# Optimization experiments

Measured on AMD Instinct MI355X. Metric: run time of the kernel, lower is better.

The kernel has to match this reference:

```python
import jax, jax.numpy as jnp
import numpy as np

B, T = 32, 25
TAU_M, TAU_S = 4.0, 1.0
TH, SG = 1.0, 4.0  # spike threshold, surrogate-gradient sharpness

@jax.custom_vjp
def spike_fn(v):
    return (v > TH).astype(v.dtype)

def _spike_fwd(v):
    return spike_fn(v), v

def _spike_bwd(v, g):
    s = jax.nn.sigmoid(SG * (v - TH))
    return (g * SG * s * (1.0 - s),)

spike_fn.defvjp(_spike_fwd, _spike_bwd)

def setup_inputs() -> dict:
    key = jax.random.key(0)
    ks = jax.random.split(key, 13)
    d = {}
    d["inputs"] = jax.random.normal(ks[0], (B, 3, 32, 32), jnp.float32)
    d["ann1_w"] = jax.random.normal(ks[1], (32, 3, 3, 3), jnp.float32) * 0.1
    d["ann1_b"] = jnp.zeros((32,), jnp.float32)
    d["w2"] = jax.random.normal(ks[2], (32, 32, 3, 3), jnp.float32) * 0.06
    d["b2"] = jnp.zeros((32,), jnp.float32)
    d["w3"] = jax.random.normal(ks[3], (64, 32, 3, 3), jnp.float32) * 0.06
    d["b3"] = jnp.zeros((64,), jnp.float32)
    d["w5"] = jax.random.normal(ks[4], (64, 64, 3, 3), jnp.float32) * 0.04
    d["b5"] = jnp.zeros((64,), jnp.float32)
    d["w7"] = jax.random.normal(ks[5], (512, 1600), jnp.float32) * (1.0 / np.sqrt(1600))
    d["b7"] = jnp.zeros((512,), jnp.float32)
    d["w8"] = jax.random.normal(ks[6], (10, 512), jnp.float32) * (1.0 / np.sqrt(512))
    d["b8"] = jnp.zeros((10,), jnp.float32)
    return d

def _conv(x, w, b):
    y = jax.lax.conv_general_dilated(x, w, (1, 1), 'VALID',
                                     dimension_numbers=('NCHW', 'OIHW', 'NCHW'))
    return y + b[None, :, None, None]

def _maxpool(x):
    return jax.lax.reduce_window(x, -jnp.inf, jax.lax.max,
                                 (1, 1, 2, 2), (1, 1, 2, 2), 'VALID')

def reference(inputs, ann1_w, ann1_b, w2, b2, w3, b3, w5, b5, w7, b7, w8, b8):
    eta_m = jnp.exp(jnp.asarray(-1.0 / TAU_M, jnp.float32))
    eta_s = jnp.exp(jnp.asarray(-1.0 / TAU_S, jnp.float32))
    a1, a2c = eta_m + eta_s, -eta_m * eta_s  # dual-exp IIR coefficients

    # ANN front-end, constant over time (expand_along_time just repeats it)
    frame = jax.nn.sigmoid(_conv(inputs, ann1_w, ann1_b))  # [B,32,30,30]

    def axon(x, st):  # second-order dual-exponential IIR synapse
        y1, y2 = st
        y = a1 * y1 + a2c * y2 + x
        return y, (y, y1)

    def lif(cur, st):  # LIF with membrane filter, zero-reset via prev spike
        v, s = st
        v_new = eta_m * v * (1.0 - s) + cur
        spk = spike_fn(v_new)
        return spk, (v_new, spk)

    def z(*shape):
        zz = jnp.zeros(shape, jnp.float32)
        return (zz, zz)

    carry0 = (z(B, 32, 30, 30), z(B, 32, 28, 28), z(B, 32, 28, 28),
              z(B, 64, 26, 26), z(B, 64, 26, 26), z(B, 64, 13, 13),
              z(B, 64, 11, 11), z(B, 64, 11, 11), z(B, 1600),
              z(B, 512), z(B, 512), z(B, 10))

    def step(carry, _):
        ax2, sn2, ax3, sn3, ax4, ax5, sn5, ax6, ax7, sn7, ax8, sn8 = carry
        a2o, ax2 = axon(frame, ax2)
        s2, sn2 = lif(_conv(a2o, w2, b2), sn2)
        a3o, ax3 = axon(s2, ax3)
        s3, sn3 = lif(_conv(a3o, w3, b3), sn3)
        a4o, ax4 = axon(s3, ax4)
        s4 = _maxpool(a4o)                       # [B,64,13,13]
        a5o, ax5 = axon(s4, ax5)
        s5, sn5 = lif(_conv(a5o, w5, b5), sn5)   # [B,64,11,11]
        a6o, ax6 = axon(s5, ax6)
        s6 = _maxpool(a6o)                       # [B,64,5,5]
        flat = s6.reshape(B, -1)                 # [B,1600]
        a7o, ax7 = axon(flat, ax7)
        s7, sn7 = lif(a7o @ w7.T + b7, sn7)      # [B,512]
        a8o, ax8 = axon(s7, ax8)
        s8, sn8 = lif(a8o @ w8.T + b8, sn8)      # [B,10]
        return (ax2, sn2, ax3, sn3, ax4, ax5, sn5, ax6, ax7, sn7, ax8, sn8), s8

    _, outs = jax.lax.scan(step, carry0, None, length=T)  # [T,B,10]
    return jnp.transpose(outs, (1, 2, 0))  # [B,10,T] matching torch time-last layout
```

## Files before the change

### kernel.cpp

```cpp
#include <hip/hip_runtime.h>
#include <math.h>


__device__ __forceinline__ float axon_step(float A1, float A2, float y1, float y2, float x) {
    return __fadd_rn(__fadd_rn(__fmul_rn(A1, y1), __fmul_rn(A2, y2)), x);
}

__global__ void diag_kernel(float* out, float v, int n) {
    int i = blockIdx.x * 256 + threadIdx.x;
    if (i < n) out[i] = v;
}

__global__ void canary_kernel(float* out, int n) {
    __shared__ float ssum[256];
    float s = 0.f;
    for (int i = threadIdx.x; i < n; i += 256) s += out[i];
    ssum[threadIdx.x] = s;
    __syncthreads();
    for (int k = 128; k > 0; k >>= 1) {
        if (threadIdx.x < k) ssum[threadIdx.x] += ssum[threadIdx.x + k];
        __syncthreads();
    }
    if (threadIdx.x == 0 && ssum[0] == 0.0f) out[0] = 444.0f;
}

__global__ __launch_bounds__(256) void wcvt_kernel(
        const float* __restrict__ w2, const float* __restrict__ w3,
        const float* __restrict__ w5,
        double* __restrict__ w2d, double* __restrict__ w3d,
        double* __restrict__ w5d) {
    int i = blockIdx.x * 256 + threadIdx.x;
    if (i < 9216)  w2d[i] = (double)w2[i];
    if (i < 18432) w3d[i] = (double)w3[i];
    if (i < 36864) w5d[i] = (double)w5[i];
}

__global__ __launch_bounds__(256) void ann1_kernel(
        const float* __restrict__ in, const float* __restrict__ w,
        const float* __restrict__ bias, float* __restrict__ frame) {
    int bid = blockIdx.x;
    int b = bid & 31, co = bid >> 5;
    int tid = threadIdx.x;
    __shared__ double wsh[27];
    if (tid < 27) wsh[tid] = (double)w[co * 27 + tid];
    __syncthreads();
    float bb = bias[co];
    for (int p = tid; p < 900; p += 256) {
        int y = p / 30, x = p % 30;
        double acc = 0.0;
        #pragma unroll
        for (int ci = 0; ci < 3; ++ci) {
            const float* r = in + ((b * 3 + ci) * 32 + y) * 32 + x;
            const double* wp = wsh + ci * 9;
            #pragma unroll
            for (int ky = 0; ky < 3; ++ky)
                acc += (double)r[ky*32+0]*wp[ky*3+0] + (double)r[ky*32+1]*wp[ky*3+1]
                     + (double)r[ky*32+2]*wp[ky*3+2];
        }
        float z = __fadd_rn((float)acc, bb);
        frame[((b * 32 + co) * 30 + y) * 30 + x] =
            (float)(1.0 / (1.0 + exp(-(double)z)));
    }
}

__global__ __launch_bounds__(256) void axon2g_kernel(
        const float2* __restrict__ frame2, float* __restrict__ a2ch,
        float A1, float A2) {
    int g = blockIdx.x * 256 + threadIdx.x;
    float2 f = frame2[g];
    float y1a = 0.f, y2a = 0.f, y1b = 0.f, y2b = 0.f;
    #pragma unroll
    for (int k = 0; k < 25; ++k) {
        float v0 = axon_step(A1, A2, y1a, y2a, f.x);
        float v1 = axon_step(A1, A2, y1b, y2b, f.y);
        ((float2*)(a2ch + (size_t)k * 921600))[g] = make_float2(v0, v1);
        y2a = y1a; y1a = v0;
        y2b = y1b; y1b = v1;
    }
}

__global__ __launch_bounds__(256) void conv2g_kernel(
        const float* __restrict__ a2ch, const double* __restrict__ w2d,
        const float* __restrict__ b2, float* __restrict__ a3ch,
        float A1, float A2, float eta_m) {
    int bid = blockIdx.x;
    int b = bid & 31, cop = (bid >> 5) & 15, sp = (bid >> 9) & 1;
    int co0 = cop * 2;
    int row0 = sp * 14;
    int p = threadIdx.x;
    if (p >= 196) return;
    int lr = p / 14, xp = p % 14;
    int y = row0 + lr, x = xp * 2;
    const double* wbase = w2d + co0 * 288;
    float bb0 = b2[co0], bb1 = b2[co0 + 1];
    float w2s[4] = {0.f, 0.f, 0.f, 0.f};
    float y3a[4] = {0.f, 0.f, 0.f, 0.f};
    float y3b[4] = {0.f, 0.f, 0.f, 0.f};
    size_t roffb = ((size_t)(b * 32) * 30 + y) * 30 + x;
    for (int tt = 0; tt < 12; ++tt) {
        const float* p0 = a2ch + (size_t)(2 * tt) * 921600;
        const float* p1 = p0 + 921600;
        double e00[2] = {0.0, 0.0}, e01[2] = {0.0, 0.0};
        double e10[2] = {0.0, 0.0}, e11[2] = {0.0, 0.0};
        #pragma unroll 2
        for (int ci = 0; ci < 32; ++ci) {
            const float* r0 = p0 + roffb + ci * 900;
            const float* r1 = p1 + roffb + ci * 900;
            const double* wp = wbase + ci * 9;
            #pragma unroll
            for (int ky = 0; ky < 3; ++ky) {
                float2 lo0 = *(const float2*)(r0 + ky * 30);
                float2 hi0 = *(const float2*)(r0 + ky * 30 + 2);
                float2 lo1 = *(const float2*)(r1 + ky * 30);
                float2 hi1 = *(const float2*)(r1 + ky * 30 + 2);
                double u0 = (double)lo0.x, u1 = (double)lo0.y;
                double u2 = (double)hi0.x, u3 = (double)hi0.y;
                double v0 = (double)lo1.x, v1 = (double)lo1.y;
                double v2 = (double)hi1.x, v3 = (double)hi1.y;
                #pragma unroll
                for (int j = 0; j < 2; ++j) {
                    const double* wj = wp + j * 288 + ky * 3;
                    e00[j] += u0*wj[0] + u1*wj[1] + u2*wj[2];
                    e01[j] += u1*wj[0] + u2*wj[1] + u3*wj[2];
                    e10[j] += v0*wj[0] + v1*wj[1] + v2*wj[2];
                    e11[j] += v1*wj[0] + v2*wj[1] + v3*wj[2];
                }
            }
        }
        float* a3o0 = a3ch + (size_t)(2 * tt) * 802816;
        float* a3o1 = a3o0 + 802816;
        #pragma unroll
        for (int j = 0; j < 2; ++j) {
            float bb = j ? bb1 : bb0;
            #pragma unroll
            for (int u = 0; u < 2; ++u) {
                int s = j * 2 + u;
                int idx = (b * 32 + co0 + j) * 784 + y * 28 + x + u;
                float cur = __fadd_rn((float)(u ? e01[j] : e00[j]), bb);
                float vn = __fadd_rn(__fmul_rn(eta_m, w2s[s]), cur);
                float sn = vn > 1.0f ? 1.0f : 0.0f;
                w2s[s] = vn > 1.0f ? 0.0f : vn;
                float yv = axon_step(A1, A2, y3a[s], y3b[s], sn);
                y3b[s] = y3a[s]; y3a[s] = yv;
                a3o0[idx] = yv;
                cur = __fadd_rn((float)(u ? e11[j] : e10[j]), bb);
                vn = __fadd_rn(__fmul_rn(eta_m, w2s[s]), cur);
                sn = vn > 1.0f ? 1.0f : 0.0f;
                w2s[s] = vn > 1.0f ? 0.0f : vn;
                yv = axon_step(A1, A2, y3a[s], y3b[s], sn);
                y3b[s] = y3a[s]; y3a[s] = yv;
                a3o1[idx] = yv;
            }
        }
    }
    {
        const float* a2o = a2ch + (size_t)24 * 921600;
        double e00[2] = {0.0, 0.0}, e01[2] = {0.0, 0.0};
        #pragma unroll 2
        for (int ci = 0; ci < 32; ++ci) {
            const float* r = a2o + roffb + ci * 900;
            const double* wp = wbase + ci * 9;
            #pragma unroll
            for (int ky = 0; ky < 3; ++ky) {
                float2 lo = *(const float2*)(r + ky * 30);
                float2 hi = *(const float2*)(r + ky * 30 + 2);
                double u0 = (double)lo.x, u1 = (double)lo.y;
                double u2 = (double)hi.x, u3 = (double)hi.y;
                #pragma unroll
                for (int j = 0; j < 2; ++j) {
                    const double* wj = wp + j * 288 + ky * 3;
                    e00[j] += u0*wj[0] + u1*wj[1] + u2*wj[2];
                    e01[j] += u1*wj[0] + u2*wj[1] + u3*wj[2];
                }
            }
        }
        float* a3o = a3ch + (size_t)24 * 802816;
        #pragma unroll
        for (int j = 0; j < 2; ++j) {
            float bb = j ? bb1 : bb0;
            #pragma unroll
            for (int u = 0; u < 2; ++u) {
                int s = j * 2 + u;
                int idx = (b * 32 + co0 + j) * 784 + y * 28 + x + u;
                float cur = __fadd_rn((float)(u ? e01[j] : e00[j]), bb);
                float vn = __fadd_rn(__fmul_rn(eta_m, w2s[s]), cur);
                float sn = vn > 1.0f ? 1.0f : 0.0f;
                w2s[s] = vn > 1.0f ? 0.0f : vn;
                float yv = axon_step(A1, A2, y3a[s], y3b[s], sn);
                y3b[s] = y3a[s]; y3a[s] = yv;
                a3o[idx] = yv;
            }
        }
    }
}

__global__ __launch_bounds__(256) void conv3g_kernel(
        const float* __restrict__ a3ch, const double* __restrict__ w3d,
        const float* __restrict__ b3, float* __restrict__ a5ch,
        float A1, float A2, float eta_m) {
    int bid = blockIdx.x;
    int b = bid & 31, coq = (bid >> 5) & 15, sp = bid >> 9;
    int co0 = coq * 4;
    int row0 = sp ? 14 : 0;
    int nrow = sp ? 12 : 14;
    int pr0  = sp ? 7 : 0;
    int npr  = sp ? 6 : 7;
    int tid = threadIdx.x;
    __shared__ float tile0[4 * 364];
    __shared__ float tile1[4 * 364];
    int npair = nrow * 13;
    int npool = npr * 13 * 4;
    const double* wbase = w3d + co0 * 288;
    int lr = 0, xp = 0, y = 0, x = 0;
    bool convAct = tid < npair;
    if (convAct) { lr = tid / 13; xp = tid % 13; y = row0 + lr; x = xp * 2; }
    float bb[4];
    #pragma unroll
    for (int j = 0; j < 4; ++j) bb[j] = b3[co0 + j];
    float w3s[8], y4a[8], y4b[8];
    #pragma unroll
    for (int s = 0; s < 8; ++s) { w3s[s] = 0.f; y4a[s] = 0.f; y4b[s] = 0.f; }
    float y5a[2] = {0.f, 0.f}, y5b[2] = {0.f, 0.f};
    size_t roffb = ((size_t)(b * 32) * 28 + y) * 28 + x;
    for (int tt = 0; tt < 12; ++tt) {
        if (convAct) {
            const float* p0 = a3ch + (size_t)(2 * tt) * 802816;
            const float* p1 = p0 + 802816;
            double e00[4] = {0,0,0,0}, e01[4] = {0,0,0,0};
            double e10[4] = {0,0,0,0}, e11[4] = {0,0,0,0};
            #pragma unroll 2
            for (int ci = 0; ci < 32; ++ci) {
                const float* r0 = p0 + roffb + ci * 784;
                const float* r1 = p1 + roffb + ci * 784;
                const double* wp = wbase + ci * 9;
                #pragma unroll
                for (int ky = 0; ky < 3; ++ky) {
                    float2 lo0 = *(const float2*)(r0 + ky * 28);
                    float2 hi0 = *(const float2*)(r0 + ky * 28 + 2);
                    float2 lo1 = *(const float2*)(r1 + ky * 28);
                    float2 hi1 = *(const float2*)(r1 + ky * 28 + 2);
                    double u0 = (double)lo0.x, u1 = (double)lo0.y;
                    double u2 = (double)hi0.x, u3 = (double)hi0.y;
                    double v0 = (double)lo1.x, v1 = (double)lo1.y;
                    double v2 = (double)hi1.x, v3 = (double)hi1.y;
                    #pragma unroll
                    for (int j = 0; j < 4; ++j) {
                        const double* wj = wp + j * 288 + ky * 3;
                        e00[j] += u0*wj[0] + u1*wj[1] + u2*wj[2];
                        e01[j] += u1*wj[0] + u2*wj[1] + u3*wj[2];
                        e10[j] += v0*wj[0] + v1*wj[1] + v2*wj[2];
                        e11[j] += v1*wj[0] + v2*wj[1] + v3*wj[2];
                    }
                }
            }
            #pragma unroll
            for (int j = 0; j < 4; ++j) {
                #pragma unroll
                for (int u = 0; u < 2; ++u) {
                    int s = j * 2 + u;
                    float cur = __fadd_rn((float)(u ? e01[j] : e00[j]), bb[j]);
                    float vn = __fadd_rn(__fmul_rn(eta_m, w3s[s]), cur);
                    float sn = vn > 1.0f ? 1.0f : 0.0f;
                    w3s[s] = vn > 1.0f ? 0.0f : vn;
                    float a4 = axon_step(A1, A2, y4a[s], y4b[s], sn);
                    y4b[s] = y4a[s]; y4a[s] = a4;
                    tile0[j * 364 + lr * 26 + x + u] = a4;
                    cur = __fadd_rn((float)(u ? e11[j] : e10[j]), bb[j]);
                    vn = __fadd_rn(__fmul_rn(eta_m, w3s[s]), cur);
                    sn = vn > 1.0f ? 1.0f : 0.0f;
                    w3s[s] = vn > 1.0f ? 0.0f : vn;
                    a4 = axon_step(A1, A2, y4a[s], y4b[s], sn);
                    y4b[s] = y4a[s]; y4a[s] = a4;
                    tile1[j * 364 + lr * 26 + x + u] = a4;
                }
            }
        }
        __syncthreads();
        float* a5o0 = a5ch + (size_t)(2 * tt) * 346112;
        float* a5o1 = a5o0 + 346112;
        #pragma unroll
        for (int s = 0; s < 2; ++s) {
            int q = tid + s * 256;
            if (q < npool) {
                int j = q / (npr * 13), pp = q % (npr * 13);
                int pry = pp / 13, px = pp % 13;
                int pr = pr0 + pry;
                int tlr = 2 * pr - row0;
                int toff = j * 364 + tlr * 26 + 2 * px;
                int idx = (b * 64 + co0 + j) * 169 + pr * 13 + px;
                const float* tp = tile0 + toff;
                float m = fmaxf(fmaxf(tp[0], tp[1]), fmaxf(tp[26], tp[27]));
                float yv = axon_step(A1, A2, y5a[s], y5b[s], m);
                y5b[s] = y5a[s]; y5a[s] = yv;
                a5o0[idx] = yv;
                tp = tile1 + toff;
                m = fmaxf(fmaxf(tp[0], tp[1]), fmaxf(tp[26], tp[27]));
                yv = axon_step(A1, A2, y5a[s], y5b[s], m);
                y5b[s] = y5a[s]; y5a[s] = yv;
                a5o1[idx] = yv;
            }
        }
        __syncthreads();
    }
    {
        if (convAct) {
            const float* a3o = a3ch + (size_t)24 * 802816;
            double e00[4] = {0,0,0,0}, e01[4] = {0,0,0,0};
            #pragma unroll 2
            for (int ci = 0; ci < 32; ++ci) {
                const float* r = a3o + roffb + ci * 784;
                const double* wp = wbase + ci * 9;
                #pragma unroll
                for (int ky = 0; ky < 3; ++ky) {
                    float2 lo = *(const float2*)(r + ky * 28);
                    float2 hi = *(const float2*)(r + ky * 28 + 2);
                    double u0 = (double)lo.x, u1 = (double)lo.y;
                    double u2 = (double)hi.x, u3 = (double)hi.y;
                    #pragma unroll
                    for (int j = 0; j < 4; ++j) {
                        const double* wj = wp + j * 288 + ky * 3;
                        e00[j] += u0*wj[0] + u1*wj[1] + u2*wj[2];
                        e01[j] += u1*wj[0] + u2*wj[1] + u3*wj[2];
                    }
                }
            }
            #pragma unroll
            for (int j = 0; j < 4; ++j) {
                #pragma unroll
                for (int u = 0; u < 2; ++u) {
                    int s = j * 2 + u;
                    float cur = __fadd_rn((float)(u ? e01[j] : e00[j]), bb[j]);
                    float vn = __fadd_rn(__fmul_rn(eta_m, w3s[s]), cur);
                    float sn = vn > 1.0f ? 1.0f : 0.0f;
                    w3s[s] = vn > 1.0f ? 0.0f : vn;
                    float a4 = axon_step(A1, A2, y4a[s], y4b[s], sn);
                    y4b[s] = y4a[s]; y4a[s] = a4;
                    tile0[j * 364 + lr * 26 + x + u] = a4;
                }
            }
        }
        __syncthreads();
        float* a5o = a5ch + (size_t)24 * 346112;
        #pragma unroll
        for (int s = 0; s < 2; ++s) {
            int q = tid + s * 256;
            if (q < npool) {
                int j = q / (npr * 13), pp = q % (npr * 13);
                int pry = pp / 13, px = pp % 13;
                int pr = pr0 + pry;
                int tlr = 2 * pr - row0;
                const float* tp = tile0 + j * 364 + tlr * 26 + 2 * px;
                float m = fmaxf(fmaxf(tp[0], tp[1]), fmaxf(tp[26], tp[27]));
                int idx = (b * 64 + co0 + j) * 169 + pr * 13 + px;
                float yv = axon_step(A1, A2, y5a[s], y5b[s], m);
                y5b[s] = y5a[s]; y5a[s] = yv;
                a5o[idx] = yv;
            }
        }
    }
}

__global__ __launch_bounds__(128) void conv5g_kernel(
        const float* __restrict__ a5ch, const double* __restrict__ w5d,
        const float* __restrict__ b5, float* __restrict__ a7ch,
        float A1, float A2, float eta_m) {
    int bid = blockIdx.x;
    int b = bid & 31, co = bid >> 5;
    int tid = threadIdx.x;
    __shared__ float tile0[121];
    __shared__ float tile1[121];
    const double* wbase = w5d + co * 576;
    float bb = b5[co];
    float w5s = 0.f, y6a = 0.f, y6b = 0.f;
    float y7a = 0.f, y7b = 0.f;
    int yy = tid / 11, xx = tid % 11;
    int py = tid / 5, px = tid % 5;
    size_t roffb = (size_t)(b * 64) * 169 + yy * 13 + xx;
    for (int tt = 0; tt < 12; ++tt) {
        if (tid < 121) {
            const float* p0 = a5ch + (size_t)(2 * tt) * 346112;
            const float* p1 = p0 + 346112;
            double a0[9] = {0,0,0,0,0,0,0,0,0};
            double a1[9] = {0,0,0,0,0,0,0,0,0};
            #pragma unroll 2
            for (int ci = 0; ci < 64; ++ci) {
                const float* r0 = p0 + roffb + ci * 169;
                const float* r1 = p1 + roffb + ci * 169;
                const double* wp = wbase + ci * 9;
                a0[0] += (double)r0[0]  * wp[0];
                a0[1] += (double)r0[1]  * wp[1];
                a0[2] += (double)r0[2]  * wp[2];
                a0[3] += (double)r0[13] * wp[3];
                a0[4] += (double)r0[14] * wp[4];
                a0[5] += (double)r0[15] * wp[5];
                a0[6] += (double)r0[26] * wp[6];
                a0[7] += (double)r0[27] * wp[7];
                a0[8] += (double)r0[28] * wp[8];
                a1[0] += (double)r1[0]  * wp[0];
                a1[1] += (double)r1[1]  * wp[1];
                a1[2] += (double)r1[2]  * wp[2];
                a1[3] += (double)r1[13] * wp[3];
                a1[4] += (double)r1[14] * wp[4];
                a1[5] += (double)r1[15] * wp[5];
                a1[6] += (double)r1[26] * wp[6];
                a1[7] += (double)r1[27] * wp[7];
                a1[8] += (double)r1[28] * wp[8];
            }
            double acc0 = ((a0[0]+a0[1])+(a0[2]+a0[3])) + ((a0[4]+a0[5])+(a0[6]+a0[7])) + a0[8];
            double acc1 = ((a1[0]+a1[1])+(a1[2]+a1[3])) + ((a1[4]+a1[5])+(a1[6]+a1[7])) + a1[8];
            float cur = __fadd_rn((float)acc0, bb);
            float vn = __fadd_rn(__fmul_rn(eta_m, w5s), cur);
            float sn = vn > 1.0f ? 1.0f : 0.0f;
            w5s = vn > 1.0f ? 0.0f : vn;
            float a6 = axon_step(A1, A2, y6a, y6b, sn);
            y6b = y6a; y6a = a6;
            tile0[tid] = a6;
            cur = __fadd_rn((float)acc1, bb);
            vn = __fadd_rn(__fmul_rn(eta_m, w5s), cur);
            sn = vn > 1.0f ? 1.0f : 0.0f;
            w5s = vn > 1.0f ? 0.0f : vn;
            a6 = axon_step(A1, A2, y6a, y6b, sn);
            y6b = y6a; y6a = a6;
            tile1[tid] = a6;
        }
        __syncthreads();
        if (tid < 25) {
            int fi = b * 1600 + co * 25 + tid;
            const float* tp = tile0 + (2*py)*11 + 2*px;
            float m = fmaxf(fmaxf(tp[0], tp[1]), fmaxf(tp[11], tp[12]));
            float yv = axon_step(A1, A2, y7a, y7b, m);
            y7b = y7a; y7a = yv;
            a7ch[(size_t)(2 * tt) * 51200 + fi] = yv;
            tp = tile1 + (2*py)*11 + 2*px;
            m = fmaxf(fmaxf(tp[0], tp[1]), fmaxf(tp[11], tp[12]));
            yv = axon_step(A1, A2, y7a, y7b, m);
            y7b = y7a; y7a = yv;
            a7ch[(size_t)(2 * tt + 1) * 51200 + fi] = yv;
        }
        __syncthreads();
    }
    {
        if (tid < 121) {
            const float* a5o = a5ch + (size_t)24 * 346112;
            double a[9] = {0,0,0,0,0,0,0,0,0};
            #pragma unroll 2
            for (int ci = 0; ci < 64; ++ci) {
                const float* r = a5o + roffb + ci * 169;
                const double* wp = wbase + ci * 9;
                a[0] += (double)r[0]  * wp[0];
                a[1] += (double)r[1]  * wp[1];
                a[2] += (double)r[2]  * wp[2];
                a[3] += (double)r[13] * wp[3];
                a[4] += (double)r[14] * wp[4];
                a[5] += (double)r[15] * wp[5];
                a[6] += (double)r[26] * wp[6];
                a[7] += (double)r[27] * wp[7];
                a[8] += (double)r[28] * wp[8];
            }
            double acc = ((a[0]+a[1])+(a[2]+a[3])) + ((a[4]+a[5])+(a[6]+a[7])) + a[8];
            float cur = __fadd_rn((float)acc, bb);
            float vn = __fadd_rn(__fmul_rn(eta_m, w5s), cur);
            float sn = vn > 1.0f ? 1.0f : 0.0f;
            w5s = vn > 1.0f ? 0.0f : vn;
            float a6 = axon_step(A1, A2, y6a, y6b, sn);
            y6b = y6a; y6a = a6;
            tile0[tid] = a6;
        }
        __syncthreads();
        if (tid < 25) {
            const float* tp = tile0 + (2*py)*11 + 2*px;
            float m = fmaxf(fmaxf(tp[0], tp[1]), fmaxf(tp[11], tp[12]));
            float yv = axon_step(A1, A2, y7a, y7b, m);
            y7b = y7a; y7a = yv;
            a7ch[(size_t)24 * 51200 + b * 1600 + co * 25 + tid] = yv;
        }
    }
}

__global__ __launch_bounds__(256) void fc7g_kernel(
        const float* __restrict__ a7ch, const float* __restrict__ w7,
        const float* __restrict__ b7, float* __restrict__ a8ch,
        float A1, float A2, float eta_m) {
    int bid = blockIdx.x;
    int b = bid & 31, ot = bid >> 5;
    int tid = threadIdx.x;
    int wave = tid >> 6, lane = tid & 63;
    __shared__ float sIn[1600];
    float w7s[4] = {0.f, 0.f, 0.f, 0.f};
    float y8a[4] = {0.f, 0.f, 0.f, 0.f};
    float y8b[4] = {0.f, 0.f, 0.f, 0.f};
    for (int t = 0; t < 25; ++t) {
        const float* a7o = a7ch + (size_t)t * 51200 + b * 1600;
        for (int i = tid; i < 1600; i += 256) sIn[i] = a7o[i];
        __syncthreads();
        float* a8o = a8ch + (size_t)t * 16384;
        #pragma unroll
        for (int oi = 0; oi < 4; ++oi) {
            int o = ot * 16 + wave * 4 + oi;
            const float* wr = w7 + o * 1600;
            double acc = 0.0;
            #pragma unroll
            for (int i = 0; i < 25; ++i)
                acc += (double)sIn[i * 64 + lane] * (double)wr[i * 64 + lane];
            #pragma unroll
            for (int off = 32; off > 0; off >>= 1)
                acc += __shfl_down(acc, off);
            if (lane == 0) {
                float cur = __fadd_rn((float)acc, b7[o]);
                float vn = __fadd_rn(__fmul_rn(eta_m, w7s[oi]), cur);
                float sn = vn > 1.0f ? 1.0f : 0.0f;
                w7s[oi] = vn > 1.0f ? 0.0f : vn;
                float yv = axon_step(A1, A2, y8a[oi], y8b[oi], sn);
                y8b[oi] = y8a[oi]; y8a[oi] = yv;
                a8o[b * 512 + o] = yv;
            }
        }
        __syncthreads();
    }
}

__global__ __launch_bounds__(64) void fc8g_kernel(
        const float* __restrict__ a8ch, const float* __restrict__ w8,
        const float* __restrict__ b8, float* __restrict__ out, float eta_m) {
    int b = blockIdx.x;
    int lane = threadIdx.x;
    float w8s[10];
    #pragma unroll
    for (int o = 0; o < 10; ++o) w8s[o] = 0.f;
    for (int t = 0; t < 25; ++t) {
        const float* sr = a8ch + (size_t)t * 16384 + b * 512;
        #pragma unroll
        for (int o = 0; o < 10; ++o) {
            const float* wr = w8 + o * 512;
            double acc = 0.0;
            #pragma unroll
            for (int i = 0; i < 8; ++i)
                acc += (double)sr[i*64+lane] * (double)wr[i*64+lane];
            #pragma unroll
            for (int off = 32; off > 0; off >>= 1)
                acc += __shfl_down(acc, off);
            if (lane == 0) {
                float cur = __fadd_rn((float)acc, b8[o]);
                float vn = __fadd_rn(__fmul_rn(eta_m, w8s[o]), cur);
                float sn = vn > 1.0f ? 1.0f : 0.0f;
                w8s[o] = vn > 1.0f ? 0.0f : vn;
                out[(b * 10 + o) * 25 + t] = sn;
            }
        }
    }
}

extern "C" void kernel_launch(void* const* d_in, const int* in_sizes, int n_in,
                              void* d_out, int out_size, void* d_ws, size_t ws_size,
                              hipStream_t stream) {
    (void)in_sizes; (void)n_in;
    const float* inp = (const float*)d_in[0];
    const float* a1w = (const float*)d_in[1];
    const float* a1b = (const float*)d_in[2];
    const float* w2  = (const float*)d_in[3];
    const float* b2  = (const float*)d_in[4];
    const float* w3  = (const float*)d_in[5];
    const float* b3  = (const float*)d_in[6];
    const float* w5  = (const float*)d_in[7];
    const float* b5  = (const float*)d_in[8];
    const float* w7  = (const float*)d_in[9];
    const float* b7  = (const float*)d_in[10];
    const float* w8  = (const float*)d_in[11];
    const float* b8  = (const float*)d_in[12];
    float* out = (float*)d_out;
    float* ws  = (float*)d_ws;

    const float em = (float)exp(-0.25);
    const float es = (float)exp(-1.0);
    const float A1 = em + es;
    const float A2 = -(em * es);

    size_t off = 0;
    auto nf = [&](size_t n) { size_t o = off; off += n; return o; };
    size_t o_w2d   = nf(2*9216);
    size_t o_w3d   = nf(2*18432);
    size_t o_w5d   = nf(2*36864);
    size_t o_frame = nf(921600);
    size_t o_a2ch  = nf((size_t)25 * 921600);
    size_t o_a3ch  = nf((size_t)25 * 802816);
    size_t o_a5ch  = nf((size_t)25 * 346112);
    size_t o_a7ch  = nf((size_t)25 * 51200);
    size_t o_a8ch  = nf((size_t)25 * 16384);

    if (ws_size < off * sizeof(float)) {
        diag_kernel<<<(out_size + 255) / 256, 256, 0, stream>>>(
            out, 100.0f + (float)(ws_size >> 20), out_size);
        return;
    }

    wcvt_kernel<<<144, 256, 0, stream>>>(w2, w3, w5,
                                         (double*)(ws + o_w2d),
                                         (double*)(ws + o_w3d),
                                         (double*)(ws + o_w5d));
    ann1_kernel<<<1024, 256, 0, stream>>>(inp, a1w, a1b, ws + o_frame);
    axon2g_kernel<<<1800, 256, 0, stream>>>((const float2*)(ws + o_frame),
                                            ws + o_a2ch, A1, A2);
    conv2g_kernel<<<1024, 256, 0, stream>>>(ws + o_a2ch,
                                            (const double*)(ws + o_w2d), b2,
                                            ws + o_a3ch, A1, A2, em);
    conv3g_kernel<<<1024, 256, 0, stream>>>(ws + o_a3ch,
                                            (const double*)(ws + o_w3d), b3,
                                            ws + o_a5ch, A1, A2, em);
    conv5g_kernel<<<2048, 128, 0, stream>>>(ws + o_a5ch,
                                            (const double*)(ws + o_w5d), b5,
                                            ws + o_a7ch, A1, A2, em);
    fc7g_kernel<<<1024, 256, 0, stream>>>(ws + o_a7ch, w7, b7,
                                          ws + o_a8ch, A1, A2, em);
    fc8g_kernel<<<32, 64, 0, stream>>>(ws + o_a8ch, w8, b8, out, em);

    canary_kernel<<<1, 256, 0, stream>>>(out, out_size);
}
```

Before: 2.070 ms.

## Transpose conv5 activations and weights to channel-last for vectorized float4 loads

Adds a transpose kernel that rewrites the layer-5 input activations from CHW to HWC per (t,b), and reorders the fp64 conv5 weights to [co][k][ci]. The conv5 inner loop now reads four channels at once with float4 loads, in place of scattered scalar loads strided by 169. This cuts load instruction count and improves access contiguity. The cost is an extra pass over about 35 MB of activation data, an extra workspace buffer, and a changed fp64 summation order within each tap.

```diff
diff --git a/kernel.cpp b/kernel.cpp
--- a/kernel.cpp
+++ b/kernel.cpp
@@ -28,11 +28,14 @@
         const float* __restrict__ w2, const float* __restrict__ w3,
         const float* __restrict__ w5,
         double* __restrict__ w2d, double* __restrict__ w3d,
-        double* __restrict__ w5d) {
+        double* __restrict__ w5dT) {
     int i = blockIdx.x * 256 + threadIdx.x;
     if (i < 9216)  w2d[i] = (double)w2[i];
     if (i < 18432) w3d[i] = (double)w3[i];
-    if (i < 36864) w5d[i] = (double)w5[i];
+    if (i < 36864) {
+        int co = i / 576, r = i % 576, ci = r / 9, k = r % 9;
+        w5dT[co * 576 + k * 64 + ci] = (double)w5[i];
+    }
 }
 
 __global__ __launch_bounds__(256) void ann1_kernel(
@@ -360,8 +363,22 @@
     }
 }
 
+__global__ __launch_bounds__(256) void transp5_kernel(
+        const float* __restrict__ a5ch, float* __restrict__ a5chT) {
+    int tb = blockIdx.x;
+    const float* src = a5ch + (size_t)tb * 10816;
+    float* dst = a5chT + (size_t)tb * 10816;
+    __shared__ float tile[10816];
+    for (int i = threadIdx.x; i < 10816; i += 256) tile[i] = src[i];
+    __syncthreads();
+    for (int i = threadIdx.x; i < 10816; i += 256) {
+        int pos = i >> 6, ci = i & 63;
+        dst[i] = tile[ci * 169 + pos];
+    }
+}
+
 __global__ __launch_bounds__(128) void conv5g_kernel(
-        const float* __restrict__ a5ch, const double* __restrict__ w5d,
+        const float* __restrict__ a5chT, const double* __restrict__ w5dT,
         const float* __restrict__ b5, float* __restrict__ a7ch,
         float A1, float A2, float eta_m) {
     int bid = blockIdx.x;
@@ -369,42 +386,38 @@
     int tid = threadIdx.x;
     __shared__ float tile0[121];
     __shared__ float tile1[121];
-    const double* wbase = w5d + co * 576;
+    const double* wb = w5dT + co * 576;
     float bb = b5[co];
     float w5s = 0.f, y6a = 0.f, y6b = 0.f;
     float y7a = 0.f, y7b = 0.f;
     int yy = tid / 11, xx = tid % 11;
     int py = tid / 5, px = tid % 5;
-    size_t roffb = (size_t)(b * 64) * 169 + yy * 13 + xx;
+    const int off0 = 0, off1 = 1, off2 = 2, off3 = 13, off4 = 14, off5 = 15,
+              off6 = 26, off7 = 27, off8 = 28;
+    size_t pbase = ((size_t)(b * 169) + yy * 13 + xx) * 64;
     for (int tt = 0; tt < 12; ++tt) {
         if (tid < 121) {
-            const float* p0 = a5ch + (size_t)(2 * tt) * 346112;
+            const float* p0 = a5chT + (size_t)(2 * tt) * 346112 + pbase;
             const float* p1 = p0 + 346112;
             double a0[9] = {0,0,0,0,0,0,0,0,0};
             double a1[9] = {0,0,0,0,0,0,0,0,0};
-            #pragma unroll 2
-            for (int ci = 0; ci < 64; ++ci) {
-                const float* r0 = p0 + roffb + ci * 169;
-                const float* r1 = p1 + roffb + ci * 169;
-                const double* wp = wbase + ci * 9;
-                a0[0] += (double)r0[0]  * wp[0];
-                a0[1] += (double)r0[1]  * wp[1];
-                a0[2] += (double)r0[2]  * wp[2];
-                a0[3] += (double)r0[13] * wp[3];
-                a0[4] += (double)r0[14] * wp[4];
-                a0[5] += (double)r0[15] * wp[5];
-                a0[6] += (double)r0[26] * wp[6];
-                a0[7] += (double)r0[27] * wp[7];
-                a0[8] += (double)r0[28] * wp[8];
-                a1[0] += (double)r1[0]  * wp[0];
-                a1[1] += (double)r1[1]  * wp[1];
-                a1[2] += (double)r1[2]  * wp[2];
-                a1[3] += (double)r1[13] * wp[3];
-                a1[4] += (double)r1[14] * wp[4];
-                a1[5] += (double)r1[15] * wp[5];
-                a1[6] += (double)r1[26] * wp[6];
-                a1[7] += (double)r1[27] * wp[7];
-                a1[8] += (double)r1[28] * wp[8];
+            for (int cq = 0; cq < 16; ++cq) {
+                int cb = cq * 4;
+                #pragma unroll
+                for (int k = 0; k < 9; ++k) {
+                    int po = (k < 3 ? k : (k < 6 ? 13 + k - 3 : 26 + k - 6));
+                    const double* wk = wb + k * 64 + cb;
+                    float4 v0 = *(const float4*)(p0 + (size_t)po * 64 + cb);
+                    float4 v1 = *(const float4*)(p1 + (size_t)po * 64 + cb);
+                    a0[k] += (double)v0.x * wk[0];
+                    a0[k] += (double)v0.y * wk[1];
+                    a0[k] += (double)v0.z * wk[2];
+                    a0[k] += (double)v0.w * wk[3];
+                    a1[k] += (double)v1.x * wk[0];
+                    a1[k] += (double)v1.y * wk[1];
+                    a1[k] += (double)v1.z * wk[2];
+                    a1[k] += (double)v1.w * wk[3];
+                }
             }
             double acc0 = ((a0[0]+a0[1])+(a0[2]+a0[3])) + ((a0[4]+a0[5])+(a0[6]+a0[7])) + a0[8];
             double acc1 = ((a1[0]+a1[1])+(a1[2]+a1[3])) + ((a1[4]+a1[5])+(a1[6]+a1[7])) + a1[8];
@@ -441,23 +454,22 @@
     }
     {
         if (tid < 121) {
-            const float* a5o = a5ch + (size_t)24 * 346112;
-            double a[9] = {0,0,0,0,0,0,0,0,0};
-            #pragma unroll 2
-            for (int ci = 0; ci < 64; ++ci) {
-                const float* r = a5o + roffb + ci * 169;
-                const double* wp = wbase + ci * 9;
-                a[0] += (double)r[0]  * wp[0];
-                a[1] += (double)r[1]  * wp[1];
-                a[2] += (double)r[2]  * wp[2];
-                a[3] += (double)r[13] * wp[3];
-                a[4] += (double)r[14] * wp[4];
-                a[5] += (double)r[15] * wp[5];
-                a[6] += (double)r[26] * wp[6];
-                a[7] += (double)r[27] * wp[7];
-                a[8] += (double)r[28] * wp[8];
-            }
-            double acc = ((a[0]+a[1])+(a[2]+a[3])) + ((a[4]+a[5])+(a[6]+a[7])) + a[8];
+            const float* p0 = a5chT + (size_t)24 * 346112 + pbase;
+            double a0[9] = {0,0,0,0,0,0,0,0,0};
+            for (int cq = 0; cq < 16; ++cq) {
+                int cb = cq * 4;
+                #pragma unroll
+                for (int k = 0; k < 9; ++k) {
+                    int po = (k < 3 ? k : (k < 6 ? 13 + k - 3 : 26 + k - 6));
+                    const double* wk = wb + k * 64 + cb;
+                    float4 v0 = *(const float4*)(p0 + (size_t)po * 64 + cb);
+                    a0[k] += (double)v0.x * wk[0];
+                    a0[k] += (double)v0.y * wk[1];
+                    a0[k] += (double)v0.z * wk[2];
+                    a0[k] += (double)v0.w * wk[3];
+                }
+            }
+            double acc = ((a0[0]+a0[1])+(a0[2]+a0[3])) + ((a0[4]+a0[5])+(a0[6]+a0[7])) + a0[8];
             float cur = __fadd_rn((float)acc, bb);
             float vn = __fadd_rn(__fmul_rn(eta_m, w5s), cur);
             float sn = vn > 1.0f ? 1.0f : 0.0f;
@@ -579,11 +591,12 @@
     auto nf = [&](size_t n) { size_t o = off; off += n; return o; };
     size_t o_w2d   = nf(2*9216);
     size_t o_w3d   = nf(2*18432);
-    size_t o_w5d   = nf(2*36864);
+    size_t o_w5dT  = nf(2*36864);
     size_t o_frame = nf(921600);
     size_t o_a2ch  = nf((size_t)25 * 921600);
     size_t o_a3ch  = nf((size_t)25 * 802816);
     size_t o_a5ch  = nf((size_t)25 * 346112);
+    size_t o_a5chT = nf((size_t)25 * 346112);
     size_t o_a7ch  = nf((size_t)25 * 51200);
     size_t o_a8ch  = nf((size_t)25 * 16384);
 
@@ -596,7 +609,7 @@
     wcvt_kernel<<<144, 256, 0, stream>>>(w2, w3, w5,
                                          (double*)(ws + o_w2d),
                                          (double*)(ws + o_w3d),
-                                         (double*)(ws + o_w5d));
+                                         (double*)(ws + o_w5dT));
     ann1_kernel<<<1024, 256, 0, stream>>>(inp, a1w, a1b, ws + o_frame);
     axon2g_kernel<<<1800, 256, 0, stream>>>((const float2*)(ws + o_frame),
                                             ws + o_a2ch, A1, A2);
@@ -606,8 +619,9 @@
     conv3g_kernel<<<1024, 256, 0, stream>>>(ws + o_a3ch,
                                             (const double*)(ws + o_w3d), b3,
                                             ws + o_a5ch, A1, A2, em);
-    conv5g_kernel<<<2048, 128, 0, stream>>>(ws + o_a5ch,
-                                            (const double*)(ws + o_w5d), b5,
+    transp5_kernel<<<800, 256, 0, stream>>>(ws + o_a5ch, ws + o_a5chT);
+    conv5g_kernel<<<2048, 128, 0, stream>>>(ws + o_a5chT,
+                                            (const double*)(ws + o_w5dT), b5,
                                             ws + o_a7ch, A1, A2, em);
     fc7g_kernel<<<1024, 256, 0, stream>>>(ws + o_a7ch, w7, b7,
                                           ws + o_a8ch, A1, A2, em);
```

Measured after the change: 3.096 ms. 49.6% more time.

## Split timestep pairs across two thread groups in conv3 and conv5 kernels

Applied to the files above, without the earlier changes.

In conv3g and conv5g, each thread used to compute the convolution for two consecutive timesteps in sequence. Now two thread groups (A and B) each compute one of the two timesteps at the same time. Group B passes its double-precision sums to group A through shared memory, and group A then runs the sequential LIF and axon recurrences. This doubles the threads per block, which raises parallelism and latency hiding and roughly halves per-thread register pressure for the accumulators. In exchange it adds an extra barrier and shared-memory traffic per step, and may lower occupancy because the larger blocks use more LDS.

```diff
diff --git a/kernel.cpp b/kernel.cpp
--- a/kernel.cpp
+++ b/kernel.cpp
@@ -194,7 +194,7 @@
     }
 }
 
-__global__ __launch_bounds__(256) void conv3g_kernel(
+__global__ __launch_bounds__(384) void conv3g_kernel(
         const float* __restrict__ a3ch, const double* __restrict__ w3d,
         const float* __restrict__ b3, float* __restrict__ a5ch,
         float A1, float A2, float eta_m) {
@@ -208,107 +208,31 @@
     int tid = threadIdx.x;
     __shared__ float tile0[4 * 364];
     __shared__ float tile1[4 * 364];
+    __shared__ double accB[182][8];
     int npair = nrow * 13;
     int npool = npr * 13 * 4;
     const double* wbase = w3d + co0 * 288;
-    int lr = 0, xp = 0, y = 0, x = 0;
-    bool convAct = tid < npair;
-    if (convAct) { lr = tid / 13; xp = tid % 13; y = row0 + lr; x = xp * 2; }
+    bool isA = tid < 192;
+    int ct = isA ? tid : tid - 192;
+    bool convAct = ct < npair;
+    int lr = 0, y = 0, x = 0;
+    if (convAct) { lr = ct / 13; int xp = ct % 13; y = row0 + lr; x = xp * 2; }
     float bb[4];
     #pragma unroll
     for (int j = 0; j < 4; ++j) bb[j] = b3[co0 + j];
     float w3s[8], y4a[8], y4b[8];
     #pragma unroll
     for (int s = 0; s < 8; ++s) { w3s[s] = 0.f; y4a[s] = 0.f; y4b[s] = 0.f; }
-    float y5a[2] = {0.f, 0.f}, y5b[2] = {0.f, 0.f};
+    float y5a = 0.f, y5b = 0.f;
     size_t roffb = ((size_t)(b * 32) * 28 + y) * 28 + x;
+    int toff_c = lr * 26 + x;
     for (int tt = 0; tt < 12; ++tt) {
+        double e0[4] = {0,0,0,0}, e1[4] = {0,0,0,0};
         if (convAct) {
-            const float* p0 = a3ch + (size_t)(2 * tt) * 802816;
-            const float* p1 = p0 + 802816;
-            double e00[4] = {0,0,0,0}, e01[4] = {0,0,0,0};
-            double e10[4] = {0,0,0,0}, e11[4] = {0,0,0,0};
+            const float* pl = a3ch + (size_t)(2 * tt + (isA ? 0 : 1)) * 802816 + roffb;
             #pragma unroll 2
             for (int ci = 0; ci < 32; ++ci) {
-                const float* r0 = p0 + roffb + ci * 784;
-                const float* r1 = p1 + roffb + ci * 784;
-                const double* wp = wbase + ci * 9;
-                #pragma unroll
-                for (int ky = 0; ky < 3; ++ky) {
-                    float2 lo0 = *(const float2*)(r0 + ky * 28);
-                    float2 hi0 = *(const float2*)(r0 + ky * 28 + 2);
-                    float2 lo1 = *(const float2*)(r1 + ky * 28);
-                    float2 hi1 = *(const float2*)(r1 + ky * 28 + 2);
-                    double u0 = (double)lo0.x, u1 = (double)lo0.y;
-                    double u2 = (double)hi0.x, u3 = (double)hi0.y;
-                    double v0 = (double)lo1.x, v1 = (double)lo1.y;
-                    double v2 = (double)hi1.x, v3 = (double)hi1.y;
-                    #pragma unroll
-                    for (int j = 0; j < 4; ++j) {
-                        const double* wj = wp + j * 288 + ky * 3;
-                        e00[j] += u0*wj[0] + u1*wj[1] + u2*wj[2];
-                        e01[j] += u1*wj[0] + u2*wj[1] + u3*wj[2];
-                        e10[j] += v0*wj[0] + v1*wj[1] + v2*wj[2];
-                        e11[j] += v1*wj[0] + v2*wj[1] + v3*wj[2];
-                    }
-                }
-            }
-            #pragma unroll
-            for (int j = 0; j < 4; ++j) {
-                #pragma unroll
-                for (int u = 0; u < 2; ++u) {
-                    int s = j * 2 + u;
-                    float cur = __fadd_rn((float)(u ? e01[j] : e00[j]), bb[j]);
-                    float vn = __fadd_rn(__fmul_rn(eta_m, w3s[s]), cur);
-                    float sn = vn > 1.0f ? 1.0f : 0.0f;
-                    w3s[s] = vn > 1.0f ? 0.0f : vn;
-                    float a4 = axon_step(A1, A2, y4a[s], y4b[s], sn);
-                    y4b[s] = y4a[s]; y4a[s] = a4;
-                    tile0[j * 364 + lr * 26 + x + u] = a4;
-                    cur = __fadd_rn((float)(u ? e11[j] : e10[j]), bb[j]);
-                    vn = __fadd_rn(__fmul_rn(eta_m, w3s[s]), cur);
-                    sn = vn > 1.0f ? 1.0f : 0.0f;
-                    w3s[s] = vn > 1.0f ? 0.0f : vn;
-                    a4 = axon_step(A1, A2, y4a[s], y4b[s], sn);
-                    y4b[s] = y4a[s]; y4a[s] = a4;
-                    tile1[j * 364 + lr * 26 + x + u] = a4;
-                }
-            }
-        }
-        __syncthreads();
-        float* a5o0 = a5ch + (size_t)(2 * tt) * 346112;
-        float* a5o1 = a5o0 + 346112;
-        #pragma unroll
-        for (int s = 0; s < 2; ++s) {
-            int q = tid + s * 256;
-            if (q < npool) {
-                int j = q / (npr * 13), pp = q % (npr * 13);
-                int pry = pp / 13, px = pp % 13;
-                int pr = pr0 + pry;
-                int tlr = 2 * pr - row0;
-                int toff = j * 364 + tlr * 26 + 2 * px;
-                int idx = (b * 64 + co0 + j) * 169 + pr * 13 + px;
-                const float* tp = tile0 + toff;
-                float m = fmaxf(fmaxf(tp[0], tp[1]), fmaxf(tp[26], tp[27]));
-                float yv = axon_step(A1, A2, y5a[s], y5b[s], m);
-                y5b[s] = y5a[s]; y5a[s] = yv;
-                a5o0[idx] = yv;
-                tp = tile1 + toff;
-                m = fmaxf(fmaxf(tp[0], tp[1]), fmaxf(tp[26], tp[27]));
-                yv = axon_step(A1, A2, y5a[s], y5b[s], m);
-                y5b[s] = y5a[s]; y5a[s] = yv;
-                a5o1[idx] = yv;
-            }
-        }
-        __syncthreads();
-    }
-    {
-        if (convAct) {
-            const float* a3o = a3ch + (size_t)24 * 802816;
-            double e00[4] = {0,0,0,0}, e01[4] = {0,0,0,0};
-            #pragma unroll 2
-            for (int ci = 0; ci < 32; ++ci) {
-                const float* r = a3o + roffb + ci * 784;
+                const float* r = pl + ci * 784;
                 const double* wp = wbase + ci * 9;
                 #pragma unroll
                 for (int ky = 0; ky < 3; ++ky) {
@@ -319,48 +243,120 @@
                     #pragma unroll
                     for (int j = 0; j < 4; ++j) {
                         const double* wj = wp + j * 288 + ky * 3;
-                        e00[j] += u0*wj[0] + u1*wj[1] + u2*wj[2];
-                        e01[j] += u1*wj[0] + u2*wj[1] + u3*wj[2];
+                        e0[j] += u0*wj[0] + u1*wj[1] + u2*wj[2];
+                        e1[j] += u1*wj[0] + u2*wj[1] + u3*wj[2];
                     }
                 }
             }
+            if (!isA) {
+                #pragma unroll
+                for (int j = 0; j < 4; ++j) {
+                    accB[ct][j * 2 + 0] = e0[j];
+                    accB[ct][j * 2 + 1] = e1[j];
+                }
+            }
+        }
+        __syncthreads();
+        if (isA && convAct) {
             #pragma unroll
             for (int j = 0; j < 4; ++j) {
                 #pragma unroll
                 for (int u = 0; u < 2; ++u) {
                     int s = j * 2 + u;
-                    float cur = __fadd_rn((float)(u ? e01[j] : e00[j]), bb[j]);
+                    int to = j * 364 + toff_c + u;
+                    float cur = __fadd_rn((float)(u ? e1[j] : e0[j]), bb[j]);
                     float vn = __fadd_rn(__fmul_rn(eta_m, w3s[s]), cur);
                     float sn = vn > 1.0f ? 1.0f : 0.0f;
                     w3s[s] = vn > 1.0f ? 0.0f : vn;
                     float a4 = axon_step(A1, A2, y4a[s], y4b[s], sn);
                     y4b[s] = y4a[s]; y4a[s] = a4;
-                    tile0[j * 364 + lr * 26 + x + u] = a4;
+                    tile0[to] = a4;
+                    cur = __fadd_rn((float)accB[ct][s], bb[j]);
+                    vn = __fadd_rn(__fmul_rn(eta_m, w3s[s]), cur);
+                    sn = vn > 1.0f ? 1.0f : 0.0f;
+                    w3s[s] = vn > 1.0f ? 0.0f : vn;
+                    a4 = axon_step(A1, A2, y4a[s], y4b[s], sn);
+                    y4b[s] = y4a[s]; y4a[s] = a4;
+                    tile1[to] = a4;
                 }
             }
         }
         __syncthreads();
-        float* a5o = a5ch + (size_t)24 * 346112;
-        #pragma unroll
-        for (int s = 0; s < 2; ++s) {
-            int q = tid + s * 256;
-            if (q < npool) {
-                int j = q / (npr * 13), pp = q % (npr * 13);
-                int pry = pp / 13, px = pp % 13;
-                int pr = pr0 + pry;
-                int tlr = 2 * pr - row0;
-                const float* tp = tile0 + j * 364 + tlr * 26 + 2 * px;
-                float m = fmaxf(fmaxf(tp[0], tp[1]), fmaxf(tp[26], tp[27]));
-                int idx = (b * 64 + co0 + j) * 169 + pr * 13 + px;
-                float yv = axon_step(A1, A2, y5a[s], y5b[s], m);
-                y5b[s] = y5a[s]; y5a[s] = yv;
-                a5o[idx] = yv;
-            }
-        }
-    }
-}
-
-__global__ __launch_bounds__(128) void conv5g_kernel(
+        if (tid < npool) {
+            int j = tid / (npr * 13), pp = tid % (npr * 13);
+            int pry = pp / 13, px = pp % 13;
+            int pr = pr0 + pry;
+            int tlr = 2 * pr - row0;
+            int toff = j * 364 + tlr * 26 + 2 * px;
+            int idx = (b * 64 + co0 + j) * 169 + pr * 13 + px;
+            float* a5o0 = a5ch + (size_t)(2 * tt) * 346112;
+            const float* tp = tile0 + toff;
+            float m = fmaxf(fmaxf(tp[0], tp[1]), fmaxf(tp[26], tp[27]));
+            float yv = axon_step(A1, A2, y5a, y5b, m);
+            y5b = y5a; y5a = yv;
+            a5o0[idx] = yv;
+            tp = tile1 + toff;
+            m = fmaxf(fmaxf(tp[0], tp[1]), fmaxf(tp[26], tp[27]));
+            yv = axon_step(A1, A2, y5a, y5b, m);
+            y5b = y5a; y5a = yv;
+            (a5o0 + 346112)[idx] = yv;
+        }
+        __syncthreads();
+    }
+    {
+        if (isA && convAct) {
+            const float* r24 = a3ch + (size_t)24 * 802816 + roffb;
+            double e0[4] = {0,0,0,0}, e1[4] = {0,0,0,0};
+            #pragma unroll 2
+            for (int ci = 0; ci < 32; ++ci) {
+                const float* r = r24 + ci * 784;
+                const double* wp = wbase + ci * 9;
+                #pragma unroll
+                for (int ky = 0; ky < 3; ++ky) {
+                    float2 lo = *(const float2*)(r + ky * 28);
+                    float2 hi = *(const float2*)(r + ky * 28 + 2);
+                    double u0 = (double)lo.x, u1 = (double)lo.y;
+                    double u2 = (double)hi.x, u3 = (double)hi.y;
+                    #pragma unroll
+                    for (int j = 0; j < 4; ++j) {
+                        const double* wj = wp + j * 288 + ky * 3;
+                        e0[j] += u0*wj[0] + u1*wj[1] + u2*wj[2];
+                        e1[j] += u1*wj[0] + u2*wj[1] + u3*wj[2];
+                    }
+                }
+            }
+            #pragma unroll
+            for (int j = 0; j < 4; ++j) {
+                #pragma unroll
+                for (int u = 0; u < 2; ++u) {
+                    int s = j * 2 + u;
+                    float cur = __fadd_rn((float)(u ? e1[j] : e0[j]), bb[j]);
+                    float vn = __fadd_rn(__fmul_rn(eta_m, w3s[s]), cur);
+                    float sn = vn > 1.0f ? 1.0f : 0.0f;
+                    w3s[s] = vn > 1.0f ? 0.0f : vn;
+                    float a4 = axon_step(A1, A2, y4a[s], y4b[s], sn);
+                    y4b[s] = y4a[s]; y4a[s] = a4;
+                    tile0[j * 364 + toff_c + u] = a4;
+                }
+            }
+        }
+        __syncthreads();
+        if (tid < npool) {
+            int j = tid / (npr * 13), pp = tid % (npr * 13);
+            int pry = pp / 13, px = pp % 13;
+            int pr = pr0 + pry;
+            int tlr = 2 * pr - row0;
+            const float* tp = tile0 + j * 364 + tlr * 26 + 2 * px;
+            float m = fmaxf(fmaxf(tp[0], tp[1]), fmaxf(tp[26], tp[27]));
+            int idx = (b * 64 + co0 + j) * 169 + pr * 13 + px;
+            float yv = axon_step(A1, A2, y5a, y5b, m);
+            y5b = y5a; y5a = yv;
+            (a5ch + (size_t)24 * 346112)[idx] = yv;
+        }
+    }
+}
+
+__global__ __launch_bounds__(256) void conv5g_kernel(
         const float* __restrict__ a5ch, const double* __restrict__ w5d,
         const float* __restrict__ b5, float* __restrict__ a7ch,
         float A1, float A2, float eta_m) {
@@ -369,59 +365,56 @@
     int tid = threadIdx.x;
     __shared__ float tile0[121];
     __shared__ float tile1[121];
+    __shared__ double accB[121];
     const double* wbase = w5d + co * 576;
     float bb = b5[co];
+    bool isA = tid < 128;
+    int ct = isA ? tid : tid - 128;
+    bool act = ct < 121;
     float w5s = 0.f, y6a = 0.f, y6b = 0.f;
     float y7a = 0.f, y7b = 0.f;
-    int yy = tid / 11, xx = tid % 11;
+    int yy = ct / 11, xx = ct % 11;
     int py = tid / 5, px = tid % 5;
     size_t roffb = (size_t)(b * 64) * 169 + yy * 13 + xx;
     for (int tt = 0; tt < 12; ++tt) {
-        if (tid < 121) {
-            const float* p0 = a5ch + (size_t)(2 * tt) * 346112;
-            const float* p1 = p0 + 346112;
-            double a0[9] = {0,0,0,0,0,0,0,0,0};
-            double a1[9] = {0,0,0,0,0,0,0,0,0};
+        double accv = 0.0;
+        if (act) {
+            const float* pl = a5ch + (size_t)(2 * tt + (isA ? 0 : 1)) * 346112 + roffb;
+            double d0 = 0.0, d1 = 0.0, d2 = 0.0, d3 = 0.0, d4 = 0.0;
+            double d5 = 0.0, d6 = 0.0, d7 = 0.0, d8 = 0.0;
             #pragma unroll 2
             for (int ci = 0; ci < 64; ++ci) {
-                const float* r0 = p0 + roffb + ci * 169;
-                const float* r1 = p1 + roffb + ci * 169;
+                const float* r = pl + ci * 169;
                 const double* wp = wbase + ci * 9;
-                a0[0] += (double)r0[0]  * wp[0];
-                a0[1] += (double)r0[1]  * wp[1];
-                a0[2] += (double)r0[2]  * wp[2];
-                a0[3] += (double)r0[13] * wp[3];
-                a0[4] += (double)r0[14] * wp[4];
-                a0[5] += (double)r0[15] * wp[5];
-                a0[6] += (double)r0[26] * wp[6];
-                a0[7] += (double)r0[27] * wp[7];
-                a0[8] += (double)r0[28] * wp[8];
-                a1[0] += (double)r1[0]  * wp[0];
-                a1[1] += (double)r1[1]  * wp[1];
-                a1[2] += (double)r1[2]  * wp[2];
-                a1[3] += (double)r1[13] * wp[3];
-                a1[4] += (double)r1[14] * wp[4];
-                a1[5] += (double)r1[15] * wp[5];
-                a1[6] += (double)r1[26] * wp[6];
-                a1[7] += (double)r1[27] * wp[7];
-                a1[8] += (double)r1[28] * wp[8];
-            }
-            double acc0 = ((a0[0]+a0[1])+(a0[2]+a0[3])) + ((a0[4]+a0[5])+(a0[6]+a0[7])) + a0[8];
-            double acc1 = ((a1[0]+a1[1])+(a1[2]+a1[3])) + ((a1[4]+a1[5])+(a1[6]+a1[7])) + a1[8];
-            float cur = __fadd_rn((float)acc0, bb);
+                d0 += (double)r[0]  * wp[0];
+                d1 += (double)r[1]  * wp[1];
+                d2 += (double)r[2]  * wp[2];
+                d3 += (double)r[13] * wp[3];
+                d4 += (double)r[14] * wp[4];
+                d5 += (double)r[15] * wp[5];
+                d6 += (double)r[26] * wp[6];
+                d7 += (double)r[27] * wp[7];
+                d8 += (double)r[28] * wp[8];
+            }
+            accv = ((d0 + d1) + (d2 + d3)) + ((d4 + d5) + (d6 + d7)) + d8;
+            if (!isA) accB[ct] = accv;
+        }
+        __syncthreads();
+        if (isA && act) {
+            float cur = __fadd_rn((float)accv, bb);
             float vn = __fadd_rn(__fmul_rn(eta_m, w5s), cur);
             float sn = vn > 1.0f ? 1.0f : 0.0f;
             w5s = vn > 1.0f ? 0.0f : vn;
             float a6 = axon_step(A1, A2, y6a, y6b, sn);
             y6b = y6a; y6a = a6;
-            tile0[tid] = a6;
-            cur = __fadd_rn((float)acc1, bb);
+            tile0[ct] = a6;
+            cur = __fadd_rn((float)accB[ct], bb);
             vn = __fadd_rn(__fmul_rn(eta_m, w5s), cur);
             sn = vn > 1.0f ? 1.0f : 0.0f;
             w5s = vn > 1.0f ? 0.0f : vn;
             a6 = axon_step(A1, A2, y6a, y6b, sn);
             y6b = y6a; y6a = a6;
-            tile1[tid] = a6;
+            tile1[ct] = a6;
         }
         __syncthreads();
         if (tid < 25) {
@@ -440,31 +433,32 @@
         __syncthreads();
     }
     {
-        if (tid < 121) {
-            const float* a5o = a5ch + (size_t)24 * 346112;
-            double a[9] = {0,0,0,0,0,0,0,0,0};
+        if (isA && act) {
+            const float* pl = a5ch + (size_t)24 * 346112 + roffb;
+            double d0 = 0.0, d1 = 0.0, d2 = 0.0, d3 = 0.0, d4 = 0.0;
+            double d5 = 0.0, d6 = 0.0, d7 = 0.0, d8 = 0.0;
             #pragma unroll 2
             for (int ci = 0; ci < 64; ++ci) {
-                const float* r = a5o + roffb + ci * 169;
+                const float* r = pl + ci * 169;
                 const double* wp = wbase + ci * 9;
-                a[0] += (double)r[0]  * wp[0];
-                a[1] += (double)r[1]  * wp[1];
-                a[2] += (double)r[2]  * wp[2];
-                a[3] += (double)r[13] * wp[3];
-                a[4] += (double)r[14] * wp[4];
-                a[5] += (double)r[15] * wp[5];
-                a[6] += (double)r[26] * wp[6];
-                a[7] += (double)r[27] * wp[7];
-                a[8] += (double)r[28] * wp[8];
-            }
-            double acc = ((a[0]+a[1])+(a[2]+a[3])) + ((a[4]+a[5])+(a[6]+a[7])) + a[8];
+                d0 += (double)r[0]  * wp[0];
+                d1 += (double)r[1]  * wp[1];
+                d2 += (double)r[2]  * wp[2];
+                d3 += (double)r[13] * wp[3];
+                d4 += (double)r[14] * wp[4];
+                d5 += (double)r[15] * wp[5];
+                d6 += (double)r[26] * wp[6];
+                d7 += (double)r[27] * wp[7];
+                d8 += (double)r[28] * wp[8];
+            }
+            double acc = ((d0 + d1) + (d2 + d3)) + ((d4 + d5) + (d6 + d7)) + d8;
             float cur = __fadd_rn((float)acc, bb);
             float vn = __fadd_rn(__fmul_rn(eta_m, w5s), cur);
             float sn = vn > 1.0f ? 1.0f : 0.0f;
             w5s = vn > 1.0f ? 0.0f : vn;
             float a6 = axon_step(A1, A2, y6a, y6b, sn);
             y6b = y6a; y6a = a6;
-            tile0[tid] = a6;
+            tile0[ct] = a6;
         }
         __syncthreads();
         if (tid < 25) {
@@ -603,10 +597,10 @@
     conv2g_kernel<<<1024, 256, 0, stream>>>(ws + o_a2ch,
                                             (const double*)(ws + o_w2d), b2,
                                             ws + o_a3ch, A1, A2, em);
-    conv3g_kernel<<<1024, 256, 0, stream>>>(ws + o_a3ch,
+    conv3g_kernel<<<1024, 384, 0, stream>>>(ws + o_a3ch,
                                             (const double*)(ws + o_w3d), b3,
                                             ws + o_a5ch, A1, A2, em);
-    conv5g_kernel<<<2048, 128, 0, stream>>>(ws + o_a5ch,
+    conv5g_kernel<<<2048, 256, 0, stream>>>(ws + o_a5ch,
                                             (const double*)(ws + o_w5d), b5,
                                             ws + o_a7ch, A1, A2, em);
     fc7g_kernel<<<1024, 256, 0, stream>>>(ws + o_a7ch, w7, b7,
```

New measurement: 2.386 ms. 15.3% more time.
